# Optimization experiments

Measured on AMD Instinct MI355X. Metric: run time of the kernel, lower is better.

Reference implementation:

```python
import jax, jax.numpy as jnp
import numpy as np

B = 16
N_IN_PER = 256
N_SKIP_PER = 1024
C_IN = 256
C_SKIP = 128


def setup_inputs() -> dict:
    key = jax.random.key(0)
    ks = jax.random.split(key, 8)
    n_in = B * N_IN_PER
    n_skip = B * N_SKIP_PER
    in_x = jax.random.normal(ks[0], (n_in, C_IN), dtype=jnp.float32)
    in_pos = jax.random.uniform(ks[1], (n_in, 3), dtype=jnp.float32)
    in_batch = jnp.repeat(jnp.arange(B, dtype=jnp.int64), N_IN_PER)
    skip_x = jax.random.normal(ks[2], (n_skip, C_SKIP), dtype=jnp.float32)
    skip_pos = jax.random.uniform(ks[3], (n_skip, 3), dtype=jnp.float32)
    skip_batch = jnp.repeat(jnp.arange(B, dtype=jnp.int64), N_SKIP_PER)
    d_cat = C_IN + C_SKIP + 3  # 387
    W1 = jax.random.normal(ks[4], (d_cat, 256), dtype=jnp.float32) * (1.0 / np.sqrt(d_cat))
    b1 = jnp.zeros((256,), dtype=jnp.float32)
    W2 = jax.random.normal(ks[5], (256, 256), dtype=jnp.float32) * (1.0 / 16.0)
    b2 = jnp.zeros((256,), dtype=jnp.float32)
    return {"in_x": in_x, "in_pos": in_pos, "in_batch": in_batch,
            "skip_x": skip_x, "skip_pos": skip_pos, "skip_batch": skip_batch,
            "W1": W1, "b1": b1, "W2": W2, "b2": b2, "knn_num": 3}


def _knn_interpolate(in_x, in_pos, in_batch, skip_pos, skip_batch, k):
    # Pairwise squared distances fine->coarse, masked across graphs. [Ns, Ni]
    d2 = jnp.sum((skip_pos[:, None, :] - in_pos[None, :, :]) ** 2, axis=-1)
    cross = skip_batch[:, None] != in_batch[None, :]
    d2 = jnp.where(cross, jnp.inf, d2)
    _, idx = jax.lax.top_k(-d2, k)  # [Ns, k] nearest coarse neighbors
    nb_pos = in_pos[idx]  # [Ns, k, 3]
    dist = jnp.sqrt(jnp.sum((nb_pos - skip_pos[:, None, :]) ** 2, axis=-1))
    dist = jnp.maximum(dist, 1e-10)
    w = 1.0 / dist
    w = w / (jnp.sum(w, axis=-1, keepdims=True) + 1e-16)  # per-target normalization
    return jnp.einsum('nk,nkc->nc', w, in_x[idx])  # [Ns, C_in]


def reference(in_x, in_pos, in_batch, skip_x, skip_pos, skip_batch, W1, b1, W2, b2, knn_num):
    interp = _knn_interpolate(in_x, in_pos, in_batch, skip_pos, skip_batch, knn_num)
    h = jnp.concatenate([interp, skip_x, skip_pos], axis=1)  # [Ns, 387]
    h = jax.nn.relu(h @ W1 + b1)
    h = jax.nn.relu(h @ W2 + b2)
    return h
```

## Files before the change

### kernel.cpp

```cpp
#include <hip/hip_runtime.h>
#include <hip/hip_bf16.h>


typedef __bf16 bf16x8 __attribute__((ext_vector_type(8)));
typedef float  f32x4  __attribute__((ext_vector_type(4)));

__device__ __forceinline__ unsigned short f2bf(float f) {
  __hip_bfloat16 h = __float2bfloat16(f);
  return __builtin_bit_cast(unsigned short, h);
}

#define GLDS16(G, L)                                                          \
  __builtin_amdgcn_global_load_lds(                                           \
      (const __attribute__((address_space(1))) void*)(G),                     \
      (__attribute__((address_space(3))) void*)(L), 16, 0, 0)

#define BAR()    __builtin_amdgcn_s_barrier()
#define WAITV(N) asm volatile("s_waitcnt vmcnt(" #N ")" ::: "memory")
#define WAITL()  asm volatile("s_waitcnt lgkmcnt(0)" ::: "memory")

static constexpr int MROWS = 16384;
static constexpr int KP1   = 448;
static constexpr int KREAL = 387;
static constexpr int NK1   = 7;
static constexpr int NK2   = 4;
static constexpr int HSTR  = 456;
static constexpr int H1STR = 264;

__global__ __launch_bounds__(256) void prep_w(
    const float* __restrict__ W1, const float* __restrict__ W2,
    unsigned short* __restrict__ W1t, unsigned short* __restrict__ W2t)
{
  __shared__ float T[64][65];
  int b = blockIdx.x;
  const float* S; unsigned short* D; int KP, Kreal, kb, nb;
  if (b < 28) { S = W1; D = W1t; KP = KP1; Kreal = KREAL; kb = b >> 2; nb = b & 3; }
  else { b -= 28; S = W2; D = W2t; KP = 256; Kreal = 256; kb = b >> 2; nb = b & 3; }
  const int k0 = kb << 6, n0 = nb << 6;
  const int tr = threadIdx.x >> 4, tc = threadIdx.x & 15;
#pragma unroll
  for (int i = 0; i < 4; ++i) {
    const int k = k0 + i * 16 + tr;
    float4 v = make_float4(0.f, 0.f, 0.f, 0.f);
    if (k < Kreal) v = *(const float4*)(S + (size_t)k * 256 + n0 + tc * 4);
    T[i * 16 + tr][tc * 4 + 0] = v.x;
    T[i * 16 + tr][tc * 4 + 1] = v.y;
    T[i * 16 + tr][tc * 4 + 2] = v.z;
    T[i * 16 + tr][tc * 4 + 3] = v.w;
  }
  __syncthreads();
#pragma unroll
  for (int i = 0; i < 4; ++i) {
    const int n = n0 + i * 16 + tr;
    const int k = k0 + tc * 4;
    ushort4 o;
    o.x = f2bf(T[tc * 4 + 0][i * 16 + tr]);
    o.y = f2bf(T[tc * 4 + 1][i * 16 + tr]);
    o.z = f2bf(T[tc * 4 + 2][i * 16 + tr]);
    o.w = f2bf(T[tc * 4 + 3][i * 16 + tr]);
    *(ushort4*)(D + (size_t)n * KP + k) = o;
  }
}

__global__ __launch_bounds__(512, 2) void fp_fused2(
    const float* __restrict__ in_x,
    const float* __restrict__ in_pos,
    const float* __restrict__ skip_x,
    const float* __restrict__ skip_pos,
    const unsigned short* __restrict__ W1t,
    const unsigned short* __restrict__ W2t,
    const float* __restrict__ bias1, const float* __restrict__ bias2,
    float* __restrict__ out)
{
  __shared__ unsigned short HU[64 * HSTR];
  __shared__ unsigned short Bs[2][256 * 64];
  __shared__ float Ps[768];

  const int tid = threadIdx.x, lane = tid & 63, wid = tid >> 6;
  const int m0 = blockIdx.x << 6;
  const int ib = (m0 >> 10) << 8;
  const int fr = lane & 15, g = lane >> 4;
  const int rg = wid >> 2, cg = wid & 3;

#define STAGEW(Wp, KW, ks, buf)                                               \
  {                                                                           \
    _Pragma("unroll")                                                         \
    for (int r_ = 0; r_ < 4; ++r_) {                                          \
      const int f_   = r_ * 512 + tid;                                        \
      const int row_ = f_ >> 3;                                               \
      const int c_   = (f_ & 7) ^ (row_ & 7);                                 \
      GLDS16(Wp + (size_t)row_ * (KW) + (ks) * 64 + c_ * 8,                   \
             &Bs[buf][(r_ * 512 + wid * 64) * 8]);                            \
    }                                                                         \
  }

  for (int i = tid; i < 768; i += 512)
    Ps[(i % 3) * 256 + i / 3] = in_pos[(size_t)ib * 3 + i];
  STAGEW(W1t, KP1, 0, 0);
  STAGEW(W1t, KP1, 1, 1);
  WAITL(); BAR();

  float Pxr[4], Pyr[4], Pzr[4];
#pragma unroll
  for (int q = 0; q < 4; ++q) {
    Pxr[q] = Ps[lane + q * 64];
    Pyr[q] = Ps[256 + lane + q * 64];
    Pzr[q] = Ps[512 + lane + q * 64];
  }
  float spv = 0.f;
  if (lane < 24) spv = skip_pos[(size_t)(m0 + wid * 8) * 3 + lane];

#pragma unroll 1
  for (int grp = 0; grp < 2; ++grp) {
    float sx[4], sy[4], sz[4], d2[4][4];
#pragma unroll
    for (int u = 0; u < 4; ++u) {
      const int pt = grp * 4 + u;
      sx[u] = __shfl(spv, 3 * pt + 0);
      sy[u] = __shfl(spv, 3 * pt + 1);
      sz[u] = __shfl(spv, 3 * pt + 2);
#pragma unroll
      for (int q = 0; q < 4; ++q) {
        const float dx = __fsub_rn(sx[u], Pxr[q]);
        const float dy = __fsub_rn(sy[u], Pyr[q]);
        const float dz = __fsub_rn(sz[u], Pzr[q]);
        d2[u][q] = __fadd_rn(__fadd_rn(__fmul_rn(dx, dx), __fmul_rn(dy, dy)),
                             __fmul_rn(dz, dz));
      }
    }
    int gsel[4][3]; float wsel[4][3], wsum[4] = {0.f, 0.f, 0.f, 0.f};
#pragma unroll
    for (int p = 0; p < 3; ++p) {
      float bd[4]; int bi[4];
#pragma unroll
      for (int u = 0; u < 4; ++u) {
        bd[u] = d2[u][0]; bi[u] = lane;
#pragma unroll
        for (int q = 1; q < 4; ++q)
          if (d2[u][q] < bd[u]) { bd[u] = d2[u][q]; bi[u] = lane + (q << 6); }
      }
#pragma unroll
      for (int mk = 1; mk < 64; mk <<= 1) {
#pragma unroll
        for (int u = 0; u < 4; ++u) {
          const float od = __shfl_xor(bd[u], mk);
          const int   oi = __shfl_xor(bi[u], mk);
          if (od < bd[u] || (od == bd[u] && oi < bi[u])) { bd[u] = od; bi[u] = oi; }
        }
      }
#pragma unroll
      for (int u = 0; u < 4; ++u) {
        const bool win = ((bi[u] & 63) == lane);
        const int  qw  = bi[u] >> 6;
        d2[u][0] = (win && qw == 0) ? 3.4e38f : d2[u][0];
        d2[u][1] = (win && qw == 1) ? 3.4e38f : d2[u][1];
        d2[u][2] = (win && qw == 2) ? 3.4e38f : d2[u][2];
        d2[u][3] = (win && qw == 3) ? 3.4e38f : d2[u][3];
        gsel[u][p] = bi[u];
        const float w = 1.0f / fmaxf(sqrtf(bd[u]), 1e-10f);
        wsel[u][p] = w; wsum[u] += w;
      }
    }
#pragma unroll
    for (int u = 0; u < 4; ++u) {
      const int lr = wid * 8 + grp * 4 + u;
      const int s  = m0 + lr;
      const float denom = wsum[u] + 1e-16f;
      const float w0 = wsel[u][0] / denom;
      const float w1 = wsel[u][1] / denom;
      const float w2 = wsel[u][2] / denom;
      const f32x4 a = *(const f32x4*)(in_x + (size_t)(ib + gsel[u][0]) * 256 + lane * 4);
      const f32x4 b = *(const f32x4*)(in_x + (size_t)(ib + gsel[u][1]) * 256 + lane * 4);
      const f32x4 c = *(const f32x4*)(in_x + (size_t)(ib + gsel[u][2]) * 256 + lane * 4);
      unsigned short* hr = &HU[lr * HSTR];
      ushort4 o4;
      o4.x = f2bf(w0 * a.x + w1 * b.x + w2 * c.x);
      o4.y = f2bf(w0 * a.y + w1 * b.y + w2 * c.y);
      o4.z = f2bf(w0 * a.z + w1 * b.z + w2 * c.z);
      o4.w = f2bf(w0 * a.w + w1 * b.w + w2 * c.w);
      *(ushort4*)(hr + lane * 4) = o4;
      const float2 sv = *(const float2*)(skip_x + (size_t)s * 128 + lane * 2);
      ushort2 o2; o2.x = f2bf(sv.x); o2.y = f2bf(sv.y);
      *(ushort2*)(hr + 256 + lane * 2) = o2;
      const float v = (lane == 0) ? sx[u] : (lane == 1) ? sy[u]
                    : (lane == 2) ? sz[u] : 0.f;
      hr[384 + lane] = f2bf(v);
    }
  }
  WAITL(); BAR();

  int Rwbase[4], Rw7[4], Rh[2];
#pragma unroll
  for (int i = 0; i < 4; ++i) {
    const int R = cg * 64 + i * 16 + fr;
    Rwbase[i] = R * 64;
    Rw7[i]    = R & 7;
  }
#pragma unroll
  for (int i = 0; i < 2; ++i) Rh[i] = rg * 32 + i * 16 + fr;

  f32x4 bv1[4], bv2[4];
#pragma unroll
  for (int mc = 0; mc < 4; ++mc) {
    bv1[mc] = *(const f32x4*)(bias1 + cg * 64 + mc * 16 + g * 4);
    bv2[mc] = *(const f32x4*)(bias2 + cg * 64 + mc * 16 + g * 4);
  }

  f32x4 acc[4][2] = {};

#pragma unroll 1
  for (int ks = 0; ks < NK1; ++ks) {
    if (ks < NK1 - 1) { WAITV(4); } else { WAITV(0); }
    BAR();
    const unsigned short* bs = Bs[ks & 1];
    bf16x8 wf[4][2], hf[2][2];
#pragma unroll
    for (int kk = 0; kk < 2; ++kk) {
#pragma unroll
      for (int i = 0; i < 4; ++i)
        wf[i][kk] = *(const bf16x8*)&bs[Rwbase[i] + (((kk * 4 + g) ^ Rw7[i]) << 3)];
#pragma unroll
      for (int i = 0; i < 2; ++i)
        hf[i][kk] = *(const bf16x8*)&HU[Rh[i] * HSTR + ks * 64 + kk * 32 + g * 8];
    }
#pragma unroll
    for (int kk = 0; kk < 2; ++kk)
#pragma unroll
      for (int mc = 0; mc < 4; ++mc)
#pragma unroll
        for (int rf = 0; rf < 2; ++rf)
          acc[mc][rf] = __builtin_amdgcn_mfma_f32_16x16x32_bf16(
              wf[mc][kk], hf[rf][kk], acc[mc][rf], 0, 0, 0);
    WAITL(); BAR();
    if (ks + 2 < NK1) STAGEW(W1t, KP1, ks + 2, ks & 1);
  }

  STAGEW(W2t, 256, 0, 0);
  STAGEW(W2t, 256, 1, 1);

  unsigned short* h1s = HU;
#pragma unroll
  for (int rf = 0; rf < 2; ++rf)
#pragma unroll
    for (int mc = 0; mc < 4; ++mc) {
      ushort4 o;
      o.x = f2bf(fmaxf(acc[mc][rf][0] + bv1[mc][0], 0.f));
      o.y = f2bf(fmaxf(acc[mc][rf][1] + bv1[mc][1], 0.f));
      o.z = f2bf(fmaxf(acc[mc][rf][2] + bv1[mc][2], 0.f));
      o.w = f2bf(fmaxf(acc[mc][rf][3] + bv1[mc][3], 0.f));
      *(ushort4*)&h1s[(rg * 32 + rf * 16 + fr) * H1STR + cg * 64 + mc * 16 + g * 4] = o;
    }
  WAITL(); BAR();

#pragma unroll
  for (int mc = 0; mc < 4; ++mc)
#pragma unroll
    for (int rf = 0; rf < 2; ++rf) acc[mc][rf] = f32x4{0.f, 0.f, 0.f, 0.f};

#pragma unroll 1
  for (int ks = 0; ks < NK2; ++ks) {
    if (ks < NK2 - 1) { WAITV(4); } else { WAITV(0); }
    BAR();
    const unsigned short* bs = Bs[ks & 1];
    bf16x8 wf[4][2], hf[2][2];
#pragma unroll
    for (int kk = 0; kk < 2; ++kk) {
#pragma unroll
      for (int i = 0; i < 4; ++i)
        wf[i][kk] = *(const bf16x8*)&bs[Rwbase[i] + (((kk * 4 + g) ^ Rw7[i]) << 3)];
#pragma unroll
      for (int i = 0; i < 2; ++i)
        hf[i][kk] = *(const bf16x8*)&h1s[Rh[i] * H1STR + ks * 64 + kk * 32 + g * 8];
    }
#pragma unroll
    for (int kk = 0; kk < 2; ++kk)
#pragma unroll
      for (int mc = 0; mc < 4; ++mc)
#pragma unroll
        for (int rf = 0; rf < 2; ++rf)
          acc[mc][rf] = __builtin_amdgcn_mfma_f32_16x16x32_bf16(
              wf[mc][kk], hf[rf][kk], acc[mc][rf], 0, 0, 0);
    WAITL(); BAR();
    if (ks + 2 < NK2) STAGEW(W2t, 256, ks + 2, ks & 1);
  }
#undef STAGEW

#pragma unroll
  for (int rf = 0; rf < 2; ++rf) {
    const size_t row = (size_t)(m0 + rg * 32 + rf * 16 + fr);
#pragma unroll
    for (int mc = 0; mc < 4; ++mc) {
      f32x4 o;
#pragma unroll
      for (int j = 0; j < 4; ++j) o[j] = fmaxf(acc[mc][rf][j] + bv2[mc][j], 0.f);
      *(f32x4*)(out + row * 256 + cg * 64 + mc * 16 + g * 4) = o;
    }
  }
}

extern "C" void kernel_launch(void* const* d_in, const int* in_sizes, int n_in,
                              void* d_out, int out_size, void* d_ws, size_t ws_size,
                              hipStream_t stream) {
  const float* in_x     = (const float*)d_in[0];
  const float* in_pos   = (const float*)d_in[1];
  const float* skip_x   = (const float*)d_in[3];
  const float* skip_pos = (const float*)d_in[4];
  const float* W1       = (const float*)d_in[6];
  const float* bias1    = (const float*)d_in[7];
  const float* W2       = (const float*)d_in[8];
  const float* bias2    = (const float*)d_in[9];

  char* ws = (char*)d_ws;
  unsigned short* W1t = (unsigned short*)(ws);
  unsigned short* W2t = (unsigned short*)(ws + 229376);

  prep_w<<<dim3(44), dim3(256), 0, stream>>>(W1, W2, W1t, W2t);
  fp_fused2<<<dim3(MROWS / 64), dim3(512), 0, stream>>>(
      in_x, in_pos, skip_x, skip_pos, W1t, W2t, bias1, bias2, (float*)d_out);
}
```

Before: 42.79 us.

## Split KNN interpolation into a prep kernel and stream H through GEMM pipeline

The fused KNN-plus-MLP kernel is split in two. A first kernel does the weight transpose and the KNN interpolation, and writes the concatenated bf16 feature matrix H to workspace. A second 256-thread GEMM kernel streams both H tiles and weight tiles into LDS with double-buffered global-to-LDS loads, and each wave computes a 64x64 output tile. This is meant to raise occupancy and overlap by removing the large per-block H buffer in LDS. The cost is an extra global round trip for H (about 14 MB of writes and reads) and a second launch.

```diff
diff --git a/kernel.cpp b/kernel.cpp
--- a/kernel.cpp
+++ b/kernel.cpp
@@ -24,276 +24,298 @@
 static constexpr int KREAL = 387;
 static constexpr int NK1   = 7;
 static constexpr int NK2   = 4;
-static constexpr int HSTR  = 456;
 static constexpr int H1STR = 264;
 
-__global__ __launch_bounds__(256) void prep_w(
-    const float* __restrict__ W1, const float* __restrict__ W2,
-    unsigned short* __restrict__ W1t, unsigned short* __restrict__ W2t)
-{
-  __shared__ float T[64][65];
-  int b = blockIdx.x;
-  const float* S; unsigned short* D; int KP, Kreal, kb, nb;
-  if (b < 28) { S = W1; D = W1t; KP = KP1; Kreal = KREAL; kb = b >> 2; nb = b & 3; }
-  else { b -= 28; S = W2; D = W2t; KP = 256; Kreal = 256; kb = b >> 2; nb = b & 3; }
-  const int k0 = kb << 6, n0 = nb << 6;
-  const int tr = threadIdx.x >> 4, tc = threadIdx.x & 15;
-#pragma unroll
-  for (int i = 0; i < 4; ++i) {
-    const int k = k0 + i * 16 + tr;
-    float4 v = make_float4(0.f, 0.f, 0.f, 0.f);
-    if (k < Kreal) v = *(const float4*)(S + (size_t)k * 256 + n0 + tc * 4);
-    T[i * 16 + tr][tc * 4 + 0] = v.x;
-    T[i * 16 + tr][tc * 4 + 1] = v.y;
-    T[i * 16 + tr][tc * 4 + 2] = v.z;
-    T[i * 16 + tr][tc * 4 + 3] = v.w;
-  }
-  __syncthreads();
-#pragma unroll
-  for (int i = 0; i < 4; ++i) {
-    const int n = n0 + i * 16 + tr;
-    const int k = k0 + tc * 4;
-    ushort4 o;
-    o.x = f2bf(T[tc * 4 + 0][i * 16 + tr]);
-    o.y = f2bf(T[tc * 4 + 1][i * 16 + tr]);
-    o.z = f2bf(T[tc * 4 + 2][i * 16 + tr]);
-    o.w = f2bf(T[tc * 4 + 3][i * 16 + tr]);
-    *(ushort4*)(D + (size_t)n * KP + k) = o;
-  }
-}
-
-__global__ __launch_bounds__(512, 2) void fp_fused2(
+__global__ __launch_bounds__(256) void knn_prep(
     const float* __restrict__ in_x,
     const float* __restrict__ in_pos,
     const float* __restrict__ skip_x,
     const float* __restrict__ skip_pos,
+    const float* __restrict__ W1, const float* __restrict__ W2,
+    unsigned short* __restrict__ W1t, unsigned short* __restrict__ W2t,
+    unsigned short* __restrict__ H)
+{
+  __shared__ float T[64][65];
+  __shared__ float P[3][256];
+  const int tid = threadIdx.x;
+
+  if (blockIdx.x < 44) {
+    int b = blockIdx.x;
+    const float* S; unsigned short* D; int KP, Kreal, kb, nb;
+    if (b < 28) { S = W1; D = W1t; KP = KP1; Kreal = KREAL; kb = b >> 2; nb = b & 3; }
+    else { b -= 28; S = W2; D = W2t; KP = 256; Kreal = 256; kb = b >> 2; nb = b & 3; }
+    const int k0 = kb << 6, n0 = nb << 6;
+    const int tr = tid >> 4, tc = tid & 15;
+#pragma unroll
+    for (int i = 0; i < 4; ++i) {
+      const int k = k0 + i * 16 + tr;
+      float4 v = make_float4(0.f, 0.f, 0.f, 0.f);
+      if (k < Kreal) v = *(const float4*)(S + (size_t)k * 256 + n0 + tc * 4);
+      T[i * 16 + tr][tc * 4 + 0] = v.x;
+      T[i * 16 + tr][tc * 4 + 1] = v.y;
+      T[i * 16 + tr][tc * 4 + 2] = v.z;
+      T[i * 16 + tr][tc * 4 + 3] = v.w;
+    }
+    __syncthreads();
+#pragma unroll
+    for (int i = 0; i < 4; ++i) {
+      const int n = n0 + i * 16 + tr;
+      const int k = k0 + tc * 4;
+      if (k < KP) {
+        ushort4 o;
+        o.x = f2bf(T[tc * 4 + 0][i * 16 + tr]);
+        o.y = f2bf(T[tc * 4 + 1][i * 16 + tr]);
+        o.z = f2bf(T[tc * 4 + 2][i * 16 + tr]);
+        o.w = f2bf(T[tc * 4 + 3][i * 16 + tr]);
+        *(ushort4*)(D + (size_t)n * KP + k) = o;
+      }
+    }
+    return;
+  }
+
+  const int s0 = (blockIdx.x - 44) << 4;
+  const int ib = (s0 >> 10) << 8;
+  {
+    const float* bp = in_pos + (size_t)ib * 3;
+    for (int i = tid; i < 768; i += 256) P[i % 3][i / 3] = bp[i];
+  }
+  __syncthreads();
+
+  const int wid = tid >> 6, lane = tid & 63;
+  const int sw = s0 + wid * 4;
+
+  float Pxr[4], Pyr[4], Pzr[4];
+#pragma unroll
+  for (int q = 0; q < 4; ++q) {
+    Pxr[q] = P[0][lane + q * 64];
+    Pyr[q] = P[1][lane + q * 64];
+    Pzr[q] = P[2][lane + q * 64];
+  }
+  float spv = 0.f;
+  if (lane < 12) spv = skip_pos[(size_t)sw * 3 + lane];
+
+  float sx[4], sy[4], sz[4], d2[4][4];
+#pragma unroll
+  for (int u = 0; u < 4; ++u) {
+    sx[u] = __shfl(spv, 3 * u + 0);
+    sy[u] = __shfl(spv, 3 * u + 1);
+    sz[u] = __shfl(spv, 3 * u + 2);
+#pragma unroll
+    for (int q = 0; q < 4; ++q) {
+      const float dx = __fsub_rn(sx[u], Pxr[q]);
+      const float dy = __fsub_rn(sy[u], Pyr[q]);
+      const float dz = __fsub_rn(sz[u], Pzr[q]);
+      d2[u][q] = __fadd_rn(__fadd_rn(__fmul_rn(dx, dx), __fmul_rn(dy, dy)),
+                           __fmul_rn(dz, dz));
+    }
+  }
+  int gsel[4][3]; float wsel[4][3], wsum[4] = {0.f, 0.f, 0.f, 0.f};
+#pragma unroll
+  for (int p = 0; p < 3; ++p) {
+    float bd[4]; int bi[4];
+#pragma unroll
+    for (int u = 0; u < 4; ++u) {
+      bd[u] = d2[u][0]; bi[u] = lane;
+#pragma unroll
+      for (int q = 1; q < 4; ++q)
+        if (d2[u][q] < bd[u]) { bd[u] = d2[u][q]; bi[u] = lane + (q << 6); }
+    }
+#pragma unroll
+    for (int mk = 1; mk < 64; mk <<= 1) {
+#pragma unroll
+      for (int u = 0; u < 4; ++u) {
+        const float od = __shfl_xor(bd[u], mk);
+        const int   oi = __shfl_xor(bi[u], mk);
+        if (od < bd[u] || (od == bd[u] && oi < bi[u])) { bd[u] = od; bi[u] = oi; }
+      }
+    }
+#pragma unroll
+    for (int u = 0; u < 4; ++u) {
+      const bool win = ((bi[u] & 63) == lane);
+      const int  qw  = bi[u] >> 6;
+      d2[u][0] = (win && qw == 0) ? 3.4e38f : d2[u][0];
+      d2[u][1] = (win && qw == 1) ? 3.4e38f : d2[u][1];
+      d2[u][2] = (win && qw == 2) ? 3.4e38f : d2[u][2];
+      d2[u][3] = (win && qw == 3) ? 3.4e38f : d2[u][3];
+      gsel[u][p] = bi[u];
+      const float w = 1.0f / fmaxf(sqrtf(bd[u]), 1e-10f);
+      wsel[u][p] = w; wsum[u] += w;
+    }
+  }
+#pragma unroll
+  for (int u = 0; u < 4; ++u) {
+    const int s = sw + u;
+    const float denom = wsum[u] + 1e-16f;
+    const float w0 = wsel[u][0] / denom;
+    const float w1 = wsel[u][1] / denom;
+    const float w2 = wsel[u][2] / denom;
+    const f32x4 a = *(const f32x4*)(in_x + (size_t)(ib + gsel[u][0]) * 256 + lane * 4);
+    const f32x4 b = *(const f32x4*)(in_x + (size_t)(ib + gsel[u][1]) * 256 + lane * 4);
+    const f32x4 c = *(const f32x4*)(in_x + (size_t)(ib + gsel[u][2]) * 256 + lane * 4);
+    unsigned short* hr = H + (size_t)s * KP1;
+    ushort4 o4;
+    o4.x = f2bf(w0 * a.x + w1 * b.x + w2 * c.x);
+    o4.y = f2bf(w0 * a.y + w1 * b.y + w2 * c.y);
+    o4.z = f2bf(w0 * a.z + w1 * b.z + w2 * c.z);
+    o4.w = f2bf(w0 * a.w + w1 * b.w + w2 * c.w);
+    *(ushort4*)(hr + (lane << 2)) = o4;
+    const float2 sv = ((const float2*)(skip_x + (size_t)s * 128))[lane];
+    ushort2 o2; o2.x = f2bf(sv.x); o2.y = f2bf(sv.y);
+    *(ushort2*)(hr + 256 + (lane << 1)) = o2;
+    const float v = (lane == 0) ? sx[u] : (lane == 1) ? sy[u]
+                  : (lane == 2) ? sz[u] : 0.f;
+    hr[384 + lane] = f2bf(v);
+  }
+}
+
+__global__ __launch_bounds__(256) void gemm12d(
+    const unsigned short* __restrict__ Hg,
     const unsigned short* __restrict__ W1t,
     const unsigned short* __restrict__ W2t,
     const float* __restrict__ bias1, const float* __restrict__ bias2,
     float* __restrict__ out)
 {
-  __shared__ unsigned short HU[64 * HSTR];
-  __shared__ unsigned short Bs[2][256 * 64];
-  __shared__ float Ps[768];
+  __shared__ unsigned short As[2][2][64 * 32];
+  __shared__ unsigned short Bs[2][2][256 * 32];
+  __shared__ unsigned short h1s[64 * H1STR];
 
   const int tid = threadIdx.x, lane = tid & 63, wid = tid >> 6;
   const int m0 = blockIdx.x << 6;
-  const int ib = (m0 >> 10) << 8;
   const int fr = lane & 15, g = lane >> 4;
-  const int rg = wid >> 2, cg = wid & 3;
-
-#define STAGEW(Wp, KW, ks, buf)                                               \
+  const int wcc = wid << 6;
+
+  const int r  = tid >> 2;
+  const int cs = (tid & 3) ^ ((r >> 1) & 3);
+  const unsigned short* gA  = Hg  + (size_t)(m0 + r) * KP1 + cs * 8;
+  const unsigned short* gB1 = W1t + (size_t)r * KP1 + cs * 8;
+  const unsigned short* gB2 = W2t + (size_t)r * 256 + cs * 8;
+
+#define STG1(ks, bu)                                                          \
   {                                                                           \
     _Pragma("unroll")                                                         \
-    for (int r_ = 0; r_ < 4; ++r_) {                                          \
-      const int f_   = r_ * 512 + tid;                                        \
-      const int row_ = f_ >> 3;                                               \
-      const int c_   = (f_ & 7) ^ (row_ & 7);                                 \
-      GLDS16(Wp + (size_t)row_ * (KW) + (ks) * 64 + c_ * 8,                   \
-             &Bs[buf][(r_ * 512 + wid * 64) * 8]);                            \
+    for (int kk_ = 0; kk_ < 2; ++kk_) {                                       \
+      const int _ko = (ks) * 64 + kk_ * 32;                                   \
+      GLDS16(gA + _ko, &As[bu][kk_][wid * 512]);                              \
+      GLDS16(gB1 + _ko,              &Bs[bu][kk_][wid * 512]);                \
+      GLDS16(gB1 + 64 * KP1 + _ko,   &Bs[bu][kk_][2048 + wid * 512]);         \
+      GLDS16(gB1 + 128 * KP1 + _ko,  &Bs[bu][kk_][4096 + wid * 512]);         \
+      GLDS16(gB1 + 192 * KP1 + _ko,  &Bs[bu][kk_][6144 + wid * 512]);         \
     }                                                                         \
   }
-
-  for (int i = tid; i < 768; i += 512)
-    Ps[(i % 3) * 256 + i / 3] = in_pos[(size_t)ib * 3 + i];
-  STAGEW(W1t, KP1, 0, 0);
-  STAGEW(W1t, KP1, 1, 1);
-  WAITL(); BAR();
-
-  float Pxr[4], Pyr[4], Pzr[4];
-#pragma unroll
-  for (int q = 0; q < 4; ++q) {
-    Pxr[q] = Ps[lane + q * 64];
-    Pyr[q] = Ps[256 + lane + q * 64];
-    Pzr[q] = Ps[512 + lane + q * 64];
-  }
-  float spv = 0.f;
-  if (lane < 24) spv = skip_pos[(size_t)(m0 + wid * 8) * 3 + lane];
-
-#pragma unroll 1
-  for (int grp = 0; grp < 2; ++grp) {
-    float sx[4], sy[4], sz[4], d2[4][4];
-#pragma unroll
-    for (int u = 0; u < 4; ++u) {
-      const int pt = grp * 4 + u;
-      sx[u] = __shfl(spv, 3 * pt + 0);
-      sy[u] = __shfl(spv, 3 * pt + 1);
-      sz[u] = __shfl(spv, 3 * pt + 2);
-#pragma unroll
-      for (int q = 0; q < 4; ++q) {
-        const float dx = __fsub_rn(sx[u], Pxr[q]);
-        const float dy = __fsub_rn(sy[u], Pyr[q]);
-        const float dz = __fsub_rn(sz[u], Pzr[q]);
-        d2[u][q] = __fadd_rn(__fadd_rn(__fmul_rn(dx, dx), __fmul_rn(dy, dy)),
-                             __fmul_rn(dz, dz));
-      }
-    }
-    int gsel[4][3]; float wsel[4][3], wsum[4] = {0.f, 0.f, 0.f, 0.f};
-#pragma unroll
-    for (int p = 0; p < 3; ++p) {
-      float bd[4]; int bi[4];
-#pragma unroll
-      for (int u = 0; u < 4; ++u) {
-        bd[u] = d2[u][0]; bi[u] = lane;
-#pragma unroll
-        for (int q = 1; q < 4; ++q)
-          if (d2[u][q] < bd[u]) { bd[u] = d2[u][q]; bi[u] = lane + (q << 6); }
-      }
-#pragma unroll
-      for (int mk = 1; mk < 64; mk <<= 1) {
-#pragma unroll
-        for (int u = 0; u < 4; ++u) {
-          const float od = __shfl_xor(bd[u], mk);
-          const int   oi = __shfl_xor(bi[u], mk);
-          if (od < bd[u] || (od == bd[u] && oi < bi[u])) { bd[u] = od; bi[u] = oi; }
-        }
-      }
-#pragma unroll
-      for (int u = 0; u < 4; ++u) {
-        const bool win = ((bi[u] & 63) == lane);
-        const int  qw  = bi[u] >> 6;
-        d2[u][0] = (win && qw == 0) ? 3.4e38f : d2[u][0];
-        d2[u][1] = (win && qw == 1) ? 3.4e38f : d2[u][1];
-        d2[u][2] = (win && qw == 2) ? 3.4e38f : d2[u][2];
-        d2[u][3] = (win && qw == 3) ? 3.4e38f : d2[u][3];
-        gsel[u][p] = bi[u];
-        const float w = 1.0f / fmaxf(sqrtf(bd[u]), 1e-10f);
-        wsel[u][p] = w; wsum[u] += w;
-      }
-    }
-#pragma unroll
-    for (int u = 0; u < 4; ++u) {
-      const int lr = wid * 8 + grp * 4 + u;
-      const int s  = m0 + lr;
-      const float denom = wsum[u] + 1e-16f;
-      const float w0 = wsel[u][0] / denom;
-      const float w1 = wsel[u][1] / denom;
-      const float w2 = wsel[u][2] / denom;
-      const f32x4 a = *(const f32x4*)(in_x + (size_t)(ib + gsel[u][0]) * 256 + lane * 4);
-      const f32x4 b = *(const f32x4*)(in_x + (size_t)(ib + gsel[u][1]) * 256 + lane * 4);
-      const f32x4 c = *(const f32x4*)(in_x + (size_t)(ib + gsel[u][2]) * 256 + lane * 4);
-      unsigned short* hr = &HU[lr * HSTR];
-      ushort4 o4;
-      o4.x = f2bf(w0 * a.x + w1 * b.x + w2 * c.x);
-      o4.y = f2bf(w0 * a.y + w1 * b.y + w2 * c.y);
-      o4.z = f2bf(w0 * a.z + w1 * b.z + w2 * c.z);
-      o4.w = f2bf(w0 * a.w + w1 * b.w + w2 * c.w);
-      *(ushort4*)(hr + lane * 4) = o4;
-      const float2 sv = *(const float2*)(skip_x + (size_t)s * 128 + lane * 2);
-      ushort2 o2; o2.x = f2bf(sv.x); o2.y = f2bf(sv.y);
-      *(ushort2*)(hr + 256 + lane * 2) = o2;
-      const float v = (lane == 0) ? sx[u] : (lane == 1) ? sy[u]
-                    : (lane == 2) ? sz[u] : 0.f;
-      hr[384 + lane] = f2bf(v);
-    }
-  }
-  WAITL(); BAR();
-
-  int Rwbase[4], Rw7[4], Rh[2];
+#define STG2(ks, bu)                                                          \
+  {                                                                           \
+    _Pragma("unroll")                                                         \
+    for (int kk_ = 0; kk_ < 2; ++kk_) {                                       \
+      const int _ko = (ks) * 64 + kk_ * 32;                                   \
+      GLDS16(gB2 + _ko,              &Bs[bu][kk_][wid * 512]);                \
+      GLDS16(gB2 + 64 * 256 + _ko,   &Bs[bu][kk_][2048 + wid * 512]);         \
+      GLDS16(gB2 + 128 * 256 + _ko,  &Bs[bu][kk_][4096 + wid * 512]);         \
+      GLDS16(gB2 + 192 * 256 + _ko,  &Bs[bu][kk_][6144 + wid * 512]);         \
+    }                                                                         \
+  }
+
+  STG1(0, 0); STG1(1, 1);
+
+  int woff[4], hoff[4], h2off[4];
 #pragma unroll
   for (int i = 0; i < 4; ++i) {
-    const int R = cg * 64 + i * 16 + fr;
-    Rwbase[i] = R * 64;
-    Rw7[i]    = R & 7;
-  }
-#pragma unroll
-  for (int i = 0; i < 2; ++i) Rh[i] = rg * 32 + i * 16 + fr;
+    const int Rw = wcc + i * 16 + fr;
+    const int Rh = i * 16 + fr;
+    woff[i]  = Rw * 32 + ((g ^ ((Rw >> 1) & 3)) << 3);
+    hoff[i]  = Rh * 32 + ((g ^ ((Rh >> 1) & 3)) << 3);
+    h2off[i] = Rh * H1STR + g * 8;
+  }
 
   f32x4 bv1[4], bv2[4];
 #pragma unroll
   for (int mc = 0; mc < 4; ++mc) {
-    bv1[mc] = *(const f32x4*)(bias1 + cg * 64 + mc * 16 + g * 4);
-    bv2[mc] = *(const f32x4*)(bias2 + cg * 64 + mc * 16 + g * 4);
-  }
-
-  f32x4 acc[4][2] = {};
+    bv1[mc] = *(const f32x4*)(bias1 + wcc + mc * 16 + g * 4);
+    bv2[mc] = *(const f32x4*)(bias2 + wcc + mc * 16 + g * 4);
+  }
+
+  f32x4 acc[4][4] = {};
 
 #pragma unroll 1
   for (int ks = 0; ks < NK1; ++ks) {
-    if (ks < NK1 - 1) { WAITV(4); } else { WAITV(0); }
+    if (ks < NK1 - 1) { WAITV(10); } else { WAITV(0); }
     BAR();
-    const unsigned short* bs = Bs[ks & 1];
-    bf16x8 wf[4][2], hf[2][2];
+    bf16x8 wf[4][2], hf[4][2];
 #pragma unroll
     for (int kk = 0; kk < 2; ++kk) {
 #pragma unroll
-      for (int i = 0; i < 4; ++i)
-        wf[i][kk] = *(const bf16x8*)&bs[Rwbase[i] + (((kk * 4 + g) ^ Rw7[i]) << 3)];
-#pragma unroll
-      for (int i = 0; i < 2; ++i)
-        hf[i][kk] = *(const bf16x8*)&HU[Rh[i] * HSTR + ks * 64 + kk * 32 + g * 8];
+      for (int i = 0; i < 4; ++i) {
+        wf[i][kk] = *(const bf16x8*)&Bs[ks & 1][kk][woff[i]];
+        hf[i][kk] = *(const bf16x8*)&As[ks & 1][kk][hoff[i]];
+      }
     }
 #pragma unroll
     for (int kk = 0; kk < 2; ++kk)
 #pragma unroll
       for (int mc = 0; mc < 4; ++mc)
 #pragma unroll
-        for (int rf = 0; rf < 2; ++rf)
-          acc[mc][rf] = __builtin_amdgcn_mfma_f32_16x16x32_bf16(
-              wf[mc][kk], hf[rf][kk], acc[mc][rf], 0, 0, 0);
+        for (int rr = 0; rr < 4; ++rr)
+          acc[mc][rr] = __builtin_amdgcn_mfma_f32_16x16x32_bf16(
+              wf[mc][kk], hf[rr][kk], acc[mc][rr], 0, 0, 0);
     WAITL(); BAR();
-    if (ks + 2 < NK1) STAGEW(W1t, KP1, ks + 2, ks & 1);
-  }
-
-  STAGEW(W2t, 256, 0, 0);
-  STAGEW(W2t, 256, 1, 1);
-
-  unsigned short* h1s = HU;
-#pragma unroll
-  for (int rf = 0; rf < 2; ++rf)
+    if (ks + 2 < NK1) STG1(ks + 2, ks & 1);
+  }
+
+  STG2(0, 0); STG2(1, 1);
+
+#pragma unroll
+  for (int rr = 0; rr < 4; ++rr)
 #pragma unroll
     for (int mc = 0; mc < 4; ++mc) {
       ushort4 o;
-      o.x = f2bf(fmaxf(acc[mc][rf][0] + bv1[mc][0], 0.f));
-      o.y = f2bf(fmaxf(acc[mc][rf][1] + bv1[mc][1], 0.f));
-      o.z = f2bf(fmaxf(acc[mc][rf][2] + bv1[mc][2], 0.f));
-      o.w = f2bf(fmaxf(acc[mc][rf][3] + bv1[mc][3], 0.f));
-      *(ushort4*)&h1s[(rg * 32 + rf * 16 + fr) * H1STR + cg * 64 + mc * 16 + g * 4] = o;
+      o.x = f2bf(fmaxf(acc[mc][rr][0] + bv1[mc][0], 0.f));
+      o.y = f2bf(fmaxf(acc[mc][rr][1] + bv1[mc][1], 0.f));
+      o.z = f2bf(fmaxf(acc[mc][rr][2] + bv1[mc][2], 0.f));
+      o.w = f2bf(fmaxf(acc[mc][rr][3] + bv1[mc][3], 0.f));
+      *(ushort4*)&h1s[(rr * 16 + fr) * H1STR + wcc + mc * 16 + g * 4] = o;
     }
   WAITL(); BAR();
 
 #pragma unroll
   for (int mc = 0; mc < 4; ++mc)
 #pragma unroll
-    for (int rf = 0; rf < 2; ++rf) acc[mc][rf] = f32x4{0.f, 0.f, 0.f, 0.f};
+    for (int rr = 0; rr < 4; ++rr) acc[mc][rr] = f32x4{0.f, 0.f, 0.f, 0.f};
 
 #pragma unroll 1
   for (int ks = 0; ks < NK2; ++ks) {
-    if (ks < NK2 - 1) { WAITV(4); } else { WAITV(0); }
+    if (ks < NK2 - 1) { WAITV(8); } else { WAITV(0); }
     BAR();
-    const unsigned short* bs = Bs[ks & 1];
-    bf16x8 wf[4][2], hf[2][2];
+    bf16x8 wf[4][2], hf[4][2];
 #pragma unroll
     for (int kk = 0; kk < 2; ++kk) {
 #pragma unroll
-      for (int i = 0; i < 4; ++i)
-        wf[i][kk] = *(const bf16x8*)&bs[Rwbase[i] + (((kk * 4 + g) ^ Rw7[i]) << 3)];
-#pragma unroll
-      for (int i = 0; i < 2; ++i)
-        hf[i][kk] = *(const bf16x8*)&h1s[Rh[i] * H1STR + ks * 64 + kk * 32 + g * 8];
+      for (int i = 0; i < 4; ++i) {
+        wf[i][kk] = *(const bf16x8*)&Bs[ks & 1][kk][woff[i]];
+        hf[i][kk] = *(const bf16x8*)&h1s[h2off[i] + ks * 64 + kk * 32];
+      }
     }
 #pragma unroll
     for (int kk = 0; kk < 2; ++kk)
 #pragma unroll
       for (int mc = 0; mc < 4; ++mc)
 #pragma unroll
-        for (int rf = 0; rf < 2; ++rf)
-          acc[mc][rf] = __builtin_amdgcn_mfma_f32_16x16x32_bf16(
-              wf[mc][kk], hf[rf][kk], acc[mc][rf], 0, 0, 0);
+        for (int rr = 0; rr < 4; ++rr)
+          acc[mc][rr] = __builtin_amdgcn_mfma_f32_16x16x32_bf16(
+              wf[mc][kk], hf[rr][kk], acc[mc][rr], 0, 0, 0);
     WAITL(); BAR();
-    if (ks + 2 < NK2) STAGEW(W2t, 256, ks + 2, ks & 1);
-  }
-#undef STAGEW
-
-#pragma unroll
-  for (int rf = 0; rf < 2; ++rf) {
-    const size_t row = (size_t)(m0 + rg * 32 + rf * 16 + fr);
+    if (ks + 2 < NK2) STG2(ks + 2, ks & 1);
+  }
+#undef STG1
+#undef STG2
+
+#pragma unroll
+  for (int rr = 0; rr < 4; ++rr) {
+    const size_t row = (size_t)(m0 + rr * 16 + fr);
 #pragma unroll
     for (int mc = 0; mc < 4; ++mc) {
       f32x4 o;
 #pragma unroll
-      for (int j = 0; j < 4; ++j) o[j] = fmaxf(acc[mc][rf][j] + bv2[mc][j], 0.f);
-      *(f32x4*)(out + row * 256 + cg * 64 + mc * 16 + g * 4) = o;
+      for (int j = 0; j < 4; ++j) o[j] = fmaxf(acc[mc][rr][j] + bv2[mc][j], 0.f);
+      *(f32x4*)(out + row * 256 + wcc + mc * 16 + g * 4) = o;
     }
   }
 }
@@ -313,8 +335,10 @@
   char* ws = (char*)d_ws;
   unsigned short* W1t = (unsigned short*)(ws);
   unsigned short* W2t = (unsigned short*)(ws + 229376);
-
-  prep_w<<<dim3(44), dim3(256), 0, stream>>>(W1, W2, W1t, W2t);
-  fp_fused2<<<dim3(MROWS / 64), dim3(512), 0, stream>>>(
-      in_x, in_pos, skip_x, skip_pos, W1t, W2t, bias1, bias2, (float*)d_out);
+  unsigned short* H   = (unsigned short*)(ws + 229376 + 131072);
+
+  knn_prep<<<dim3(44 + MROWS / 16), dim3(256), 0, stream>>>(
+      in_x, in_pos, skip_x, skip_pos, W1, W2, W1t, W2t, H);
+  gemm12d<<<dim3(MROWS / 64), dim3(256), 0, stream>>>(
+      H, W1t, W2t, bias1, bias2, (float*)d_out);
 }
```

New measurement: 41.14 us. 1.04x faster.
